# Optimization experiments

Hardware: AMD Instinct MI355X
Metric: run time of the kernel (lower is better)

Reference implementation:

```python
import jax, jax.numpy as jnp
import numpy as np

FEAT = [(200, 200), (100, 100), (50, 50), (25, 25), (13, 13)]
STRIDES = [4, 8, 16, 32, 64]
SIZES = [32, 64, 128, 256, 512]
RATIOS = np.array([0.5, 1.0, 2.0])
NUM_PER_LEVEL = [h * w * 3 for h, w in FEAT]  # [120000,30000,7500,1875,507]
A_TOTAL = sum(NUM_PER_LEVEL)                  # 159882
B = 4
IMG_H = IMG_W = 800.0
PRE_NMS = 1000      # pre_nms_top_n['testing'] (per level)
POST_NMS = 1000     # post_nms_top_n['testing']
NMS_T = 0.7
SCORE_T = 0.0
MIN_SIZE = 0.001
BBOX_CLIP = float(np.log(1000.0 / 16.0))  # torchvision bbox_xform_clip
LVL_OFFSET = 1000.0                       # > max image coord, for batched_nms trick
LVL_FULL = jnp.asarray(np.repeat(np.arange(5), NUM_PER_LEVEL))  # [A_TOTAL]


def _make_anchors():
    out = []
    for (fh, fw), stride, size in zip(FEAT, STRIDES, SIZES):
        ws = np.sqrt(size * size / RATIOS)
        hs = ws * RATIOS
        base = np.stack([-ws / 2, -hs / 2, ws / 2, hs / 2], axis=1)  # [3,4]
        sx = (np.arange(fw) + 0.5) * stride
        sy = (np.arange(fh) + 0.5) * stride
        cy, cx = np.meshgrid(sy, sx, indexing='ij')
        shifts = np.stack([cx, cy, cx, cy], axis=-1).reshape(-1, 1, 4)
        out.append((shifts + base[None]).reshape(-1, 4))
    return np.concatenate(out, 0).astype(np.float32)


def setup_inputs() -> dict:
    key = jax.random.key(0)
    k1, k2 = jax.random.split(key)
    objectness = jax.random.normal(k1, (B, A_TOTAL), jnp.float32)
    pred_bbox_deltas = jax.random.normal(k2, (B, A_TOTAL, 4), jnp.float32) * 0.5
    anchors = jnp.asarray(_make_anchors())  # real FPN anchor grid [A_TOTAL,4]
    return {"objectness": objectness, "pred_bbox_deltas": pred_bbox_deltas, "anchors": anchors}


def _decode(deltas, anchors):
    # torchvision BoxCoder.decode with weights (1,1,1,1)
    wa = anchors[:, 2] - anchors[:, 0]
    ha = anchors[:, 3] - anchors[:, 1]
    cxa = anchors[:, 0] + 0.5 * wa
    cya = anchors[:, 1] + 0.5 * ha
    dx, dy = deltas[..., 0], deltas[..., 1]
    dw = jnp.minimum(deltas[..., 2], BBOX_CLIP)
    dh = jnp.minimum(deltas[..., 3], BBOX_CLIP)
    cx = dx * wa + cxa
    cy = dy * ha + cya
    w = jnp.exp(dw) * wa
    h = jnp.exp(dh) * ha
    return jnp.stack([cx - 0.5 * w, cy - 0.5 * h, cx + 0.5 * w, cy + 0.5 * h], axis=-1)


def _pairwise_iou(b):
    area = (b[:, 2] - b[:, 0]) * (b[:, 3] - b[:, 1])
    lt = jnp.maximum(b[:, None, :2], b[None, :, :2])
    rb = jnp.minimum(b[:, None, 2:], b[None, :, 2:])
    wh = jnp.clip(rb - lt, 0.0)
    inter = wh[..., 0] * wh[..., 1]
    return inter / (area[:, None] + area[None, :] - inter)


def _nms_image(boxes, scores, lvl):
    # boxes [K,4], scores [K], lvl [K] -> fixed-size [POST_NMS,5] = (x1,y1,x2,y2,score)
    K = boxes.shape[0]
    sg = jax.lax.stop_gradient
    x1 = jnp.clip(boxes[:, 0], 0.0, IMG_W)
    y1 = jnp.clip(boxes[:, 1], 0.0, IMG_H)
    x2 = jnp.clip(boxes[:, 2], 0.0, IMG_W)
    y2 = jnp.clip(boxes[:, 3], 0.0, IMG_H)
    boxes = jnp.stack([x1, y1, x2, y2], axis=1)
    # remove_small_boxes + score threshold
    valid = (sg(x2 - x1) >= MIN_SIZE) & (sg(y2 - y1) >= MIN_SIZE) & (sg(scores) >= SCORE_T)
    order = jnp.argsort(-jnp.where(valid, sg(scores), -jnp.inf))
    boxes = boxes[order]
    scores = scores[order]
    lvl = lvl[order]
    valid = valid[order]
    # batched_nms trick: offset boxes per level so cross-level IoU is 0
    off = sg(boxes) + (lvl.astype(boxes.dtype) * LVL_OFFSET)[:, None]
    iou = _pairwise_iou(off)  # [K,K], decision-only (stop_gradient)
    idx = jnp.arange(K)
    def body(i, keep):
        sup = (iou[i] > NMS_T) & keep[i] & (idx > i)
        return keep & (~sup)
    keep = jax.lax.fori_loop(0, K, body, valid)
    rank = jnp.cumsum(keep) - 1
    sel = keep & (rank < POST_NMS)
    rows = jnp.concatenate([boxes, scores[:, None]], axis=1)
    dst = jnp.where(sel, rank, POST_NMS)  # out-of-range rows dropped
    out = jnp.zeros((POST_NMS, 5), boxes.dtype)
    return out.at[dst].set(jnp.where(sel[:, None], rows, 0.0), mode="drop")


def reference(objectness, pred_bbox_deltas, anchors):
    proposals = _decode(pred_bbox_deltas, anchors)  # [B, A_TOTAL, 4]
    # per-level top-k on objectness logits
    idx_list = []
    off = 0
    for n in NUM_PER_LEVEL:
        k = min(PRE_NMS, n)
        _, ti = jax.lax.top_k(objectness[:, off:off + n], k)
        idx_list.append(ti + off)
        off += n
    top_idx = jnp.concatenate(idx_list, axis=1)  # [B, K=4507]
    obj_k = jnp.take_along_axis(objectness, top_idx, axis=1)
    boxes_k = jnp.take_along_axis(proposals, top_idx[..., None], axis=1)
    lvl_k = LVL_FULL[top_idx]
    scores_k = jax.nn.sigmoid(obj_k)
    # clip + small-box filter + score filter + batched NMS + post-nms topk, per image
    return jax.vmap(_nms_image)(boxes_k, scores_k, lvl_k)  # [B, POST_NMS, 5]
```

## Files before the change

### kernel.cpp

```cpp
#include <hip/hip_runtime.h>
#include <stdint.h>

#define KTOT 4507
#define POSTN 1000
#define ATOT 159882
#define NIMG 4
#define CAND_CAP 4096
#define SLOTCAP 5000
#define BPI 22
#define MT_IMG 73728


__device__ inline unsigned fmono(float f) {
    unsigned u = __float_as_uint(f);
    return (u & 0x80000000u) ? ~u : (u | 0x80000000u);
}
__device__ inline float fmono_inv(unsigned u) {
    unsigned b = (u & 0x80000000u) ? (u ^ 0x80000000u) : ~u;
    return __uint_as_float(b);
}

__device__ inline unsigned long long shfl_u64(unsigned long long v, int src) {
    int lo = __shfl((int)(unsigned)(v & 0xFFFFFFFFULL), src);
    int hi = __shfl((int)(unsigned)(v >> 32), src);
    return ((unsigned long long)(unsigned)hi << 32) | (unsigned)lo;
}

__device__ inline void async16(unsigned long long* lds, const unsigned long long* g) {
#if __has_builtin(__builtin_amdgcn_global_load_lds)
    __builtin_amdgcn_global_load_lds(
        (const __attribute__((address_space(1))) unsigned*)g,
        (__attribute__((address_space(3))) unsigned*)lds, 16, 0, 0);
#else
    *(ulonglong2*)lds = *(const ulonglong2*)g;
#endif
}

__device__ inline int blockExclScan(int v, int* warpSums) {
    int tid = threadIdx.x;
    int lane = tid & 63, wid = tid >> 6;
    int x = v;
#pragma unroll
    for (int d = 1; d < 64; d <<= 1) {
        int y = __shfl_up(x, d);
        if (lane >= d) x += y;
    }
    if (lane == 63) warpSums[wid] = x;
    __syncthreads();
    if (wid == 0) {
        int s = (lane < 16) ? warpSums[lane] : 0;
#pragma unroll
        for (int d = 1; d < 16; d <<= 1) {
            int y = __shfl_up(s, d);
            if (lane >= d) s += y;
        }
        if (lane < 16) warpSums[lane] = s;
    }
    __syncthreads();
    int wpre = (wid == 0) ? 0 : warpSums[wid - 1];
    return wpre + (x - v);
}

__device__ __constant__ int c_lvlOff[5] = {0, 120000, 150000, 157500, 159375};
__device__ __constant__ int c_lvlN[5]   = {120000, 30000, 7500, 1875, 507};
__device__ __constant__ int c_slsz[5]   = {8000, 7500, 7500, 1875, 507};
__device__ __constant__ int c_blvl[BPI] = {0,0,0,0,0,0,0,0,0,0,0,0,0,0,0, 1,1,1,1, 2, 3, 4};
__device__ __constant__ int c_bsl[BPI]  = {0,1,2,3,4,5,6,7,8,9,10,11,12,13,14, 0,1,2,3, 0, 0, 0};
__device__ __constant__ int c_bstart[5] = {0, 15, 19, 20, 21};
__device__ __constant__ int c_bcnt[5]   = {15, 4, 1, 1, 1};

__device__ inline size_t mtBase(int img, int lvl) {
    return (size_t)img * MT_IMG + (lvl < 4 ? (size_t)lvl * 16384 : 65536);
}


__global__ __launch_bounds__(1024) void hist_kernel(const float* __restrict__ obj,
                                                    unsigned* __restrict__ ghist) {
    __shared__ unsigned hist[4096];
    int img = blockIdx.x / BPI, b = blockIdx.x % BPI;
    int lvl = c_blvl[b], sl = c_bsl[b];
    int n = c_lvlN[lvl];
    int s0 = sl * c_slsz[lvl];
    int send = min(s0 + c_slsz[lvl], n);
    const float* src = obj + (size_t)img * ATOT + c_lvlOff[lvl];
    int tid = threadIdx.x;

    for (int i = tid; i < 4096; i += 1024) hist[i] = 0u;
    __syncthreads();

    int base = s0 + tid, last = send - 1;
    float v0 = src[min(base,        last)];
    float v1 = src[min(base + 1024, last)];
    float v2 = src[min(base + 2048, last)];
    float v3 = src[min(base + 3072, last)];
    float v4 = src[min(base + 4096, last)];
    float v5 = src[min(base + 5120, last)];
    float v6 = src[min(base + 6144, last)];
    float v7 = src[min(base + 7168, last)];
#define HIST1(U, VV) if (base + (U)*1024 < send) atomicAdd(&hist[fmono(VV) >> 20], 1u);
    HIST1(0, v0) HIST1(1, v1) HIST1(2, v2) HIST1(3, v3)
    HIST1(4, v4) HIST1(5, v5) HIST1(6, v6) HIST1(7, v7)
#undef HIST1
    __syncthreads();

    unsigned* gh = ghist + (size_t)(img * BPI + b) * 4096;
    for (int i = tid; i < 4096; i += 1024) gh[i] = hist[i];
}


__global__ __launch_bounds__(1024) void gather_kernel(const float* __restrict__ obj,
                                                      const unsigned* __restrict__ ghist,
                                                      unsigned long long* __restrict__ gcand,
                                                      int* __restrict__ gcnt,
                                                      int* __restrict__ gbstar) {
    __shared__ int s_misc[32];
    __shared__ int s_bstar, s_cnt;
    int img = blockIdx.x / BPI, b = blockIdx.x % BPI;
    int lvl = c_blvl[b], sl = c_bsl[b];
    int seg = img * BPI + b;
    int n = c_lvlN[lvl];
    int k = (lvl == 4) ? 507 : 1000;
    int s0 = sl * c_slsz[lvl];
    int send = min(s0 + c_slsz[lvl], n);
    const float* src = obj + (size_t)img * ATOT + c_lvlOff[lvl];
    int tid = threadIdx.x;
    int lane = tid & 63;

    if (tid == 0) s_cnt = 0;

    unsigned hx = 0, hy = 0, hz = 0, hw = 0;
    {
        int bs = c_bstart[lvl], bc = c_bcnt[lvl];
        for (int s = 0; s < bc; s++) {
            const uint4* gh4 = (const uint4*)(ghist + (size_t)(img * BPI + bs + s) * 4096);
            uint4 t = gh4[tid];
            hx += t.x; hy += t.y; hz += t.z; hw += t.w;
        }
    }
    int mysum = (int)(hx + hy + hz + hw);
    int excl = blockExclScan(mysum, s_misc);
    int target = n - k;
    {
        int P = excl;
        if ((int)hx > 0 && P <= target && target < P + (int)hx) s_bstar = 4 * tid + 0;
        P += (int)hx;
        if ((int)hy > 0 && P <= target && target < P + (int)hy) s_bstar = 4 * tid + 1;
        P += (int)hy;
        if ((int)hz > 0 && P <= target && target < P + (int)hz) s_bstar = 4 * tid + 2;
        P += (int)hz;
        if ((int)hw > 0 && P <= target && target < P + (int)hw) s_bstar = 4 * tid + 3;
    }
    __syncthreads();
    int bstar = s_bstar;
    if (tid == 0 && sl == 0) gbstar[img * 5 + lvl] = bstar;

    unsigned long long* gc = gcand + (size_t)seg * CAND_CAP;
    int base = s0 + tid, last = send - 1;
    float v0 = src[min(base,        last)];
    float v1 = src[min(base + 1024, last)];
    float v2 = src[min(base + 2048, last)];
    float v3 = src[min(base + 3072, last)];
    float v4 = src[min(base + 4096, last)];
    float v5 = src[min(base + 5120, last)];
    float v6 = src[min(base + 6144, last)];
    float v7 = src[min(base + 7168, last)];
#define PUSH1(U, VV)                                                                     \
    {                                                                                    \
        int ix = base + (U) * 1024;                                                      \
        unsigned key = fmono(VV);                                                        \
        bool s = (ix < send) && ((int)(key >> 20) >= bstar);                             \
        unsigned long long mk = __ballot(s);                                             \
        if (mk) {                                                                        \
            int pre = __popcll(mk & ((1ULL << lane) - 1ULL));                            \
            int ldr = __builtin_ctzll(mk);                                               \
            int basew = 0;                                                               \
            if (lane == ldr) basew = atomicAdd(&s_cnt, __popcll(mk));                    \
            basew = __shfl(basew, ldr);                                                  \
            if (s) {                                                                     \
                int pos = basew + pre;                                                   \
                if (pos < CAND_CAP)                                                      \
                    gc[pos] = ((unsigned long long)key << 32) | (unsigned)(~(unsigned)ix); \
            }                                                                            \
        }                                                                                \
    }
    PUSH1(0, v0) PUSH1(1, v1) PUSH1(2, v2) PUSH1(3, v3)
    PUSH1(4, v4) PUSH1(5, v5) PUSH1(6, v6) PUSH1(7, v7)
#undef PUSH1
    __syncthreads();
    if (tid == 0) gcnt[seg] = min(s_cnt, CAND_CAP);
}


__global__ __launch_bounds__(1024) void rankdecode_kernel(
    const float* __restrict__ deltas, const float* __restrict__ anchors,
    const unsigned long long* __restrict__ gcand, const int* __restrict__ gcnt,
    const int* __restrict__ gbstar,
    float* __restrict__ sx1, float* __restrict__ sy1, float* __restrict__ sx2,
    float* __restrict__ sy2, float* __restrict__ sscore,
    float* __restrict__ cx1, float* __restrict__ cy1, float* __restrict__ cx2,
    float* __restrict__ cy2, float* __restrict__ car,
    unsigned long long* __restrict__ ckey, int* __restrict__ cslot, int* __restrict__ cm) {
    __shared__ unsigned long long ck[CAND_CAP];
    __shared__ __attribute__((aligned(16))) unsigned subh[4096];
    __shared__ int s_warp[32];
    __shared__ int s_tot, s_sub, s_m2;

    int grp = blockIdx.x;
    int img = grp / 5, lvl = grp % 5;
    int kn = (lvl == 4) ? 507 : 1000;
    int koff = lvl * 1000;
    int tid = threadIdx.x;

    int bs = c_bstart[lvl], bc = c_bcnt[lvl];
    int pref = 0;
    for (int s = 0; s < bc; s++) {
        int c = gcnt[img * BPI + bs + s];
        const unsigned long long* segp = gcand + (size_t)(img * BPI + bs + s) * CAND_CAP;
        for (int i = tid; i < c; i += 1024) {
            int d = pref + i;
            if (d < CAND_CAP) ck[d] = segp[i];
        }
        pref += c;
    }
    int m = min(pref, CAND_CAP);
    int bstarv = gbstar[grp];
    __syncthreads();

    int mm = m;
    if (m > 1024) {
        for (int i = tid; i < 4096; i += 1024) subh[i] = 0u;
        __syncthreads();
        int c0 = tid, c1 = tid + 1024, c2 = tid + 2048, c3 = tid + 3072;
        unsigned long long e0 = (c0 < m) ? ck[c0] : 0ULL;
        unsigned long long e1 = (c1 < m) ? ck[c1] : 0ULL;
        unsigned long long e2 = (c2 < m) ? ck[c2] : 0ULL;
        unsigned long long e3 = (c3 < m) ? ck[c3] : 0ULL;
        int hiCnt = 0;
#define CLS(E, C)                                                                        \
        if ((C) < m) {                                                                   \
            if ((unsigned)((E) >> 52) > (unsigned)bstarv) hiCnt++;                       \
            else atomicAdd(&subh[(unsigned)(((E) >> 40) & 0xFFFULL)], 1u);               \
        }
        CLS(e0, c0) CLS(e1, c1) CLS(e2, c2) CLS(e3, c3)
#undef CLS
        int exH = blockExclScan(hiCnt, s_warp);
        if (tid == 1023) s_tot = exH + hiCnt;
        __syncthreads();
        int cntHi = s_tot;
        int target2 = (m - cntHi) - (kn - cntHi);
        const uint4* sh4 = (const uint4*)subh;
        uint4 sc = sh4[tid];
        int ms2 = (int)(sc.x + sc.y + sc.z + sc.w);
        int ex2 = blockExclScan(ms2, s_warp);
        {
            int Pp = ex2;
            if ((int)sc.x > 0 && Pp <= target2 && target2 < Pp + (int)sc.x) s_sub = 4 * tid + 0;
            Pp += (int)sc.x;
            if ((int)sc.y > 0 && Pp <= target2 && target2 < Pp + (int)sc.y) s_sub = 4 * tid + 1;
            Pp += (int)sc.y;
            if ((int)sc.z > 0 && Pp <= target2 && target2 < Pp + (int)sc.z) s_sub = 4 * tid + 2;
            Pp += (int)sc.z;
            if ((int)sc.w > 0 && Pp <= target2 && target2 < Pp + (int)sc.w) s_sub = 4 * tid + 3;
        }
        __syncthreads();
        int cstar = s_sub;
#define FLG(E, C)                                                                        \
        (((C) < m) && (((unsigned)((E) >> 52) > (unsigned)bstarv) ||                     \
                       ((unsigned)(((E) >> 40) & 0xFFFULL) >= (unsigned)cstar)))
        int f0 = FLG(e0, c0), f1 = FLG(e1, c1), f2 = FLG(e2, c2), f3 = FLG(e3, c3);
#undef FLG
        int fc = f0 + f1 + f2 + f3;
        int pos = blockExclScan(fc, s_warp);
        if (tid == 1023) s_m2 = pos + fc;
        __syncthreads();
        int m2 = s_m2;
        if (m2 <= 1024) {
            int p = pos;
            if (f0) ck[p++] = e0;
            if (f1) ck[p++] = e1;
            if (f2) ck[p++] = e2;
            if (f3) ck[p++] = e3;
            mm = m2;
        }
        __syncthreads();
    }

    int P = 512;
    while (P < mm) P <<= 1;
    for (int i = mm + tid; i < P; i += 1024) ck[i] = 0ULL;
    __syncthreads();

    for (unsigned kk = 2; kk <= (unsigned)P; kk <<= 1) {
        for (unsigned j = kk >> 1; j > 0; j >>= 1) {
            for (unsigned i = (unsigned)tid; i < (unsigned)P; i += 1024) {
                unsigned ixj = i ^ j;
                if (ixj > i) {
                    unsigned long long a = ck[i], b2 = ck[ixj];
                    bool up = ((i & kk) == 0);
                    if ((a > b2) == up) { ck[i] = b2; ck[ixj] = a; }
                }
            }
            __syncthreads();
        }
    }

    int r = tid;
    size_t o = (size_t)img * KTOT + koff + r;
    float x1 = 0.f, y1 = 0.f, x2 = 0.f, y2 = 0.f, s = 0.f;
    int valid = 0;
    if (r < kn) {
        unsigned long long key = ck[P - 1 - r];
        int idx = c_lvlOff[lvl] + (int)(~(unsigned)key);
        float logit = fmono_inv((unsigned)(key >> 32));
        float ef = (float)exp(-(double)logit);
        s = 1.0f / __fadd_rn(1.0f, ef);
        float a0 = anchors[(size_t)idx * 4 + 0], a1 = anchors[(size_t)idx * 4 + 1];
        float a2 = anchors[(size_t)idx * 4 + 2], a3 = anchors[(size_t)idx * 4 + 3];
        const float* dp = deltas + ((size_t)img * ATOT + idx) * 4;
        float dx = dp[0], dy = dp[1];
        const float BCLIP = 4.135166556742356f;
        float dw = fminf(dp[2], BCLIP), dh = fminf(dp[3], BCLIP);
        float wa = __fsub_rn(a2, a0), ha = __fsub_rn(a3, a1);
        float cxa = __fadd_rn(a0, __fmul_rn(0.5f, wa));
        float cya = __fadd_rn(a1, __fmul_rn(0.5f, ha));
        float cx = __fadd_rn(__fmul_rn(dx, wa), cxa);
        float cy = __fadd_rn(__fmul_rn(dy, ha), cya);
        float w = __fmul_rn((float)exp((double)dw), wa);
        float h = __fmul_rn((float)exp((double)dh), ha);
        x1 = __fsub_rn(cx, __fmul_rn(0.5f, w));
        y1 = __fsub_rn(cy, __fmul_rn(0.5f, h));
        x2 = __fadd_rn(cx, __fmul_rn(0.5f, w));
        y2 = __fadd_rn(cy, __fmul_rn(0.5f, h));
        x1 = fminf(fmaxf(x1, 0.0f), 800.0f);
        y1 = fminf(fmaxf(y1, 0.0f), 800.0f);
        x2 = fminf(fmaxf(x2, 0.0f), 800.0f);
        y2 = fminf(fmaxf(y2, 0.0f), 800.0f);
        valid = (__fsub_rn(x2, x1) >= 0.001f) && (__fsub_rn(y2, y1) >= 0.001f) && (s >= 0.0f);
        sx1[o] = x1; sy1[o] = y1; sx2[o] = x2; sy2[o] = y2; sscore[o] = s;
    }

    int pos = blockExclScan(valid, s_warp);
    if (valid) {
        float lf = 1000.0f * (float)lvl;
        size_t cb = (size_t)img * SLOTCAP + koff + pos;
        float ox1 = __fadd_rn(x1, lf);
        float oy1 = __fadd_rn(y1, lf);
        float ox2 = __fadd_rn(x2, lf);
        float oy2 = __fadd_rn(y2, lf);
        cx1[cb] = ox1; cy1[cb] = oy1; cx2[cb] = ox2; cy2[cb] = oy2;
        car[cb] = __fmul_rn(__fsub_rn(ox2, ox1), __fsub_rn(oy2, oy1));
        int p = koff + r;
        ckey[cb] = ((unsigned long long)fmono(s) << 32) | (unsigned)(~(unsigned)p);
        cslot[cb] = p;
    }
    if (tid == 1023) cm[grp] = pos + valid;
}


__global__ __launch_bounds__(512) void mask_kernel(
    const float* __restrict__ cx1, const float* __restrict__ cy1,
    const float* __restrict__ cx2, const float* __restrict__ cy2,
    const float* __restrict__ car, const int* __restrict__ cm,
    unsigned long long* __restrict__ maskT) {
    __shared__ float lx1[1000], ly1[1000], lx2[1000], ly2[1000], lar[1000];
    int iq = blockIdx.y;
    int img = iq / 5, lvl = iq % 5;
    int m = cm[iq];
    int W = (m + 63) >> 6;
    int T = (W * (W + 1)) >> 1;
    int tbase = blockIdx.x * 8;
    if (tbase >= T) return;

    size_t cb0 = (size_t)img * SLOTCAP + lvl * 1000;
    for (int q = threadIdx.x; q < m; q += 512) {
        lx1[q] = cx1[cb0 + q]; ly1[q] = cy1[cb0 + q];
        lx2[q] = cx2[cb0 + q]; ly2[q] = cy2[cb0 + q];
        lar[q] = car[cb0 + q];
    }
    __syncthreads();

    int wv = threadIdx.x >> 6, lane = threadIdx.x & 63;
    int t = tbase + wv;
    if (t >= T) return;
    int w = (int)((sqrtf(8.0f * (float)t + 1.0f) - 1.0f) * 0.5f);
    while (((w + 1) * (w + 2)) / 2 <= t) w++;
    while ((w * (w + 1)) / 2 > t) w--;
    int c = t - ((w * (w + 1)) >> 1);

    unsigned long long* MT = maskT + mtBase(img, lvl);

    int j = (w << 6) + lane;
    bool jv = j < m;
    float jx1 = jv ? lx1[j] : 0.f, jy1 = jv ? ly1[j] : 0.f;
    float jx2 = jv ? lx2[j] : 0.f, jy2 = jv ? ly2[j] : 0.f;
    float jar = jv ? lar[j] : 0.f;

    unsigned long long myword = 0ULL;
    int i0 = c << 6, i1 = min(i0 + 64, m);
    for (int i = i0; i < i1; i++) {
        float ix1 = lx1[i], iy1 = ly1[i], ix2 = lx2[i], iy2 = ly2[i], iar = lar[i];
        float ltx = fmaxf(ix1, jx1);
        float lty = fmaxf(iy1, jy1);
        float rbx = fminf(ix2, jx2);
        float rby = fminf(iy2, jy2);
        float wq = fmaxf(__fsub_rn(rbx, ltx), 0.0f);
        float hq = fmaxf(__fsub_rn(rby, lty), 0.0f);
        float inter = __fmul_rn(wq, hq);
        float uni = __fsub_rn(__fadd_rn(iar, jar), inter);
        float iou = inter / uni;
        bool bit = jv && (j > i) && (iou > 0.7f);
        unsigned long long bal = __ballot(bit);
        if (lane == (i & 63)) myword = bal;
    }
    int irow = i0 + lane;
    if (irow < i1) MT[(size_t)irow * 16 + w] = myword;
}


__global__ __launch_bounds__(256, 1) void scan_kernel(
    const unsigned long long* __restrict__ maskT, const int* __restrict__ cm,
    unsigned long long* __restrict__ keepWords) {
    __shared__ unsigned long long M[16384];
    __shared__ unsigned long long s_alive[16], s_kill[16];
    __shared__ int s_go;
    int grp = blockIdx.x;
    int img = grp / 5, lvl = grp % 5;
    int m = cm[grp];
    int tid = threadIdx.x;
    int wv = tid >> 6, lane = tid & 63;
    int w16 = lane & 15, g = lane >> 4;
    int rowgrp = wv * 4 + g;

    if (m == 0) {
        if (tid < 16) keepWords[grp * 16 + tid] = 0ULL;
        return;
    }

    const unsigned long long* src = maskT + mtBase(img, lvl);
    int rounds = (m * 16 + 511) >> 9;
    for (int k = 0; k < rounds; k++) {
        int u = (k << 9) + tid * 2;
        async16(&M[u], &src[u]);
    }
    int fw = m >> 6, tb = m & 63;
    if (tid < 16) {
        unsigned long long a = (tid < fw) ? ~0ULL
                              : (tid == fw && tb) ? ((1ULL << tb) - 1ULL) : 0ULL;
        s_alive[tid] = a;
        s_kill[tid] = 0ULL;
    }
    if (tid == 0) s_go = 1;
    __syncthreads();

    for (int it = 0; it <= m && s_go; it++) {
        unsigned long long p = 0ULL;
        for (int r = rowgrp; r < m; r += 16) {
            unsigned long long aw = s_alive[r >> 6];
            unsigned long long bit = (aw >> (r & 63)) & 1ULL;
            bit &= (unsigned long long)(w16 >= (r >> 6));
            p |= M[r * 16 + w16] & (0ULL - bit);
        }
        p |= shfl_u64(p, (lane + 32) & 63);
        p |= shfl_u64(p, (lane + 16) & 63);
        if (lane < 16 && p) atomicOr(&s_kill[lane], p);
        __syncthreads();
        if (wv == 0) {
            unsigned long long neww = 0ULL, oldw = 0ULL;
            if (lane < 16) {
                unsigned long long initw = (lane < fw) ? ~0ULL
                                          : (lane == fw && tb) ? ((1ULL << tb) - 1ULL) : 0ULL;
                oldw = s_alive[lane];
                neww = initw & ~s_kill[lane];
                s_alive[lane] = neww;
                s_kill[lane] = 0ULL;
            }
            unsigned long long ch = __ballot(lane < 16 && neww != oldw);
            if (lane == 0) s_go = (ch != 0ULL) ? 1 : 0;
        }
        __syncthreads();
    }
    if (tid < 16) keepWords[grp * 16 + tid] = s_alive[tid];
}


__global__ __launch_bounds__(1024) void scanout_kernel(
    const float* __restrict__ sx1, const float* __restrict__ sy1,
    const float* __restrict__ sx2, const float* __restrict__ sy2,
    const float* __restrict__ sscore,
    const unsigned long long* __restrict__ ckey, const int* __restrict__ cslot,
    const unsigned long long* __restrict__ keepWords, float* __restrict__ out) {
    __shared__ unsigned long long kkey[SLOTCAP];
    __shared__ int kslot[SLOTCAP];
    __shared__ int s_warp[32];
    __shared__ int s_pref[6];
    __shared__ int s_cnt[5];

    int img = blockIdx.x, tid = threadIdx.x;

    int f[5];
    int e0 = tid * 5;
    int cnt = 0;
#pragma unroll
    for (int c = 0; c < 5; c++) {
        int e = e0 + c;
        int fl = 0;
        if (e < 5000) {
            int lvl = e / 1000, rr = e - lvl * 1000;
            fl = (int)((keepWords[(img * 5 + lvl) * 16 + (rr >> 6)] >> (rr & 63)) & 1ULL);
        }
        f[c] = fl;
        cnt += fl;
    }
    int pos = blockExclScan(cnt, s_warp);
    {
        int run = pos;
#pragma unroll
        for (int c = 0; c < 5; c++) {
            int e = e0 + c;
            if (e < 5000 && (e - (e / 1000) * 1000) == 0) s_pref[e / 1000] = run;
            run += f[c];
        }
    }
    if (tid == 1023) s_pref[5] = pos + cnt;
    __syncthreads();
    {
        int run = pos;
#pragma unroll
        for (int c = 0; c < 5; c++) {
            int e = e0 + c;
            if (f[c]) {
                int lvl = e / 1000, rr = e - lvl * 1000;
                int pil = run - s_pref[lvl];
                size_t cb = (size_t)img * SLOTCAP + lvl * 1000 + rr;
                kkey[lvl * 1000 + pil] = ckey[cb];
                kslot[lvl * 1000 + pil] = cslot[cb];
            }
            run += f[c];
        }
    }
    if (tid < 5) s_cnt[tid] = s_pref[tid + 1] - s_pref[tid];
    __syncthreads();

    int tK = s_pref[5];

    for (int lvl = 0; lvl < 5; lvl++) {
        int Kc = s_cnt[lvl];
        int koff = lvl * 1000;
        for (int q = tid; q < Kc; q += 1024) {
            unsigned long long key = kkey[koff + q];
            int rank = q;
#pragma unroll
            for (int ol = 0; ol < 5; ol++) {
                if (ol == lvl) continue;
                int lo = 0, hi = s_cnt[ol], base = ol * 1000;
                while (lo < hi) {
                    int mid = (lo + hi) >> 1;
                    if (kkey[base + mid] > key) lo = mid + 1; else hi = mid;
                }
                rank += lo;
            }
            if (rank < POSTN) {
                int slot = kslot[koff + q];
                size_t o = (size_t)img * KTOT + slot;
                float* dst = out + ((size_t)img * POSTN + rank) * 5;
                dst[0] = sx1[o]; dst[1] = sy1[o]; dst[2] = sx2[o]; dst[3] = sy2[o];
                dst[4] = sscore[o];
            }
        }
    }

    int z0 = tK < POSTN ? tK : POSTN;
    int nz = (POSTN - z0) * 5;
    float* ob = out + (size_t)img * POSTN * 5 + (size_t)z0 * 5;
    for (int u = tid; u < nz; u += 1024) ob[u] = 0.f;
}


extern "C" void kernel_launch(void* const* d_in, const int* in_sizes, int n_in,
                              void* d_out, int out_size, void* d_ws, size_t ws_size,
                              hipStream_t stream) {
    const float* obj = (const float*)d_in[0];
    const float* deltas = (const float*)d_in[1];
    const float* anchors = (const float*)d_in[2];
    float* out = (float*)d_out;

    char* ws = (char*)d_ws;
    size_t off = 0;
    auto alloc = [&](size_t bytes) {
        size_t o = off;
        off += (bytes + 255) & ~(size_t)255;
        return o;
    };
    unsigned* ghist = (unsigned*)(ws + alloc((size_t)NIMG * BPI * 4096 * 4));
    int* gcnt = (int*)(ws + alloc((size_t)NIMG * BPI * 4));
    int* gbstar = (int*)(ws + alloc((size_t)NIMG * 5 * 4));
    unsigned long long* gcand =
        (unsigned long long*)(ws + alloc((size_t)NIMG * BPI * CAND_CAP * 8));
    float* sx1 = (float*)(ws + alloc((size_t)NIMG * KTOT * 4));
    float* sy1 = (float*)(ws + alloc((size_t)NIMG * KTOT * 4));
    float* sx2 = (float*)(ws + alloc((size_t)NIMG * KTOT * 4));
    float* sy2 = (float*)(ws + alloc((size_t)NIMG * KTOT * 4));
    float* sscore = (float*)(ws + alloc((size_t)NIMG * KTOT * 4));
    float* cx1 = (float*)(ws + alloc((size_t)NIMG * SLOTCAP * 4));
    float* cy1 = (float*)(ws + alloc((size_t)NIMG * SLOTCAP * 4));
    float* cx2 = (float*)(ws + alloc((size_t)NIMG * SLOTCAP * 4));
    float* cy2 = (float*)(ws + alloc((size_t)NIMG * SLOTCAP * 4));
    float* car = (float*)(ws + alloc((size_t)NIMG * SLOTCAP * 4));
    unsigned long long* ckey = (unsigned long long*)(ws + alloc((size_t)NIMG * SLOTCAP * 8));
    int* cslot = (int*)(ws + alloc((size_t)NIMG * SLOTCAP * 4));
    int* cm = (int*)(ws + alloc((size_t)NIMG * 5 * 4));
    unsigned long long* maskT = (unsigned long long*)(ws + alloc((size_t)NIMG * MT_IMG * 8));
    unsigned long long* keepWords = (unsigned long long*)(ws + alloc((size_t)NIMG * 5 * 16 * 8));

    hist_kernel<<<dim3(NIMG * BPI), dim3(1024), 0, stream>>>(obj, ghist);
    gather_kernel<<<dim3(NIMG * BPI), dim3(1024), 0, stream>>>(obj, ghist, gcand, gcnt,
                                                               gbstar);
    rankdecode_kernel<<<dim3(NIMG * 5), dim3(1024), 0, stream>>>(
        deltas, anchors, gcand, gcnt, gbstar, sx1, sy1, sx2, sy2, sscore,
        cx1, cy1, cx2, cy2, car, ckey, cslot, cm);
    mask_kernel<<<dim3(17, NIMG * 5), dim3(512), 0, stream>>>(cx1, cy1, cx2, cy2, car, cm,
                                                              maskT);
    scan_kernel<<<dim3(NIMG * 5), dim3(256), 0, stream>>>(maskT, cm, keepWords);
    scanout_kernel<<<dim3(NIMG), dim3(1024), 0, stream>>>(
        sx1, sy1, sx2, sy2, sscore, ckey, cslot, keepWords, out);
}
```

Baseline: 163.1 us.

## Fuse rank/decode, IoU mask build, and NMS scan into one per-level kernel

Measured after the change: 265.7 us. 62.9% more time.

```diff
diff --git a/kernel.cpp b/kernel.cpp
--- a/kernel.cpp
+++ b/kernel.cpp
@@ -8,7 +8,6 @@
 #define CAND_CAP 4096
 #define SLOTCAP 5000
 #define BPI 22
-#define MT_IMG 73728
 
 
 __device__ inline unsigned fmono(float f) {
@@ -24,16 +23,6 @@
     int lo = __shfl((int)(unsigned)(v & 0xFFFFFFFFULL), src);
     int hi = __shfl((int)(unsigned)(v >> 32), src);
     return ((unsigned long long)(unsigned)hi << 32) | (unsigned)lo;
-}
-
-__device__ inline void async16(unsigned long long* lds, const unsigned long long* g) {
-#if __has_builtin(__builtin_amdgcn_global_load_lds)
-    __builtin_amdgcn_global_load_lds(
-        (const __attribute__((address_space(1))) unsigned*)g,
-        (__attribute__((address_space(3))) unsigned*)lds, 16, 0, 0);
-#else
-    *(ulonglong2*)lds = *(const ulonglong2*)g;
-#endif
 }
 
 __device__ inline int blockExclScan(int v, int* warpSums) {
@@ -68,10 +57,6 @@
 __device__ __constant__ int c_bsl[BPI]  = {0,1,2,3,4,5,6,7,8,9,10,11,12,13,14, 0,1,2,3, 0, 0, 0};
 __device__ __constant__ int c_bstart[5] = {0, 15, 19, 20, 21};
 __device__ __constant__ int c_bcnt[5]   = {15, 4, 1, 1, 1};
-
-__device__ inline size_t mtBase(int img, int lvl) {
-    return (size_t)img * MT_IMG + (lvl < 4 ? (size_t)lvl * 16384 : 65536);
-}
 
 
 __global__ __launch_bounds__(1024) void hist_kernel(const float* __restrict__ obj,
@@ -191,25 +176,29 @@
 }
 
 
-__global__ __launch_bounds__(1024) void rankdecode_kernel(
+__global__ __launch_bounds__(1024, 1) void mega_kernel(
     const float* __restrict__ deltas, const float* __restrict__ anchors,
     const unsigned long long* __restrict__ gcand, const int* __restrict__ gcnt,
     const int* __restrict__ gbstar,
     float* __restrict__ sx1, float* __restrict__ sy1, float* __restrict__ sx2,
     float* __restrict__ sy2, float* __restrict__ sscore,
-    float* __restrict__ cx1, float* __restrict__ cy1, float* __restrict__ cx2,
-    float* __restrict__ cy2, float* __restrict__ car,
-    unsigned long long* __restrict__ ckey, int* __restrict__ cslot, int* __restrict__ cm) {
-    __shared__ unsigned long long ck[CAND_CAP];
-    __shared__ __attribute__((aligned(16))) unsigned subh[4096];
+    unsigned long long* __restrict__ ckey, int* __restrict__ cslot,
+    unsigned long long* __restrict__ keepWords) {
+    __shared__ __attribute__((aligned(16))) unsigned long long M[16384];
+    __shared__ float lx1[1024], ly1[1024], lx2[1024], ly2[1024], lar[1024];
     __shared__ int s_warp[32];
-    __shared__ int s_tot, s_sub, s_m2;
+    __shared__ unsigned long long s_alive[16], s_kill[16];
+    __shared__ int s_go, s_m, s_tot, s_sub, s_m2;
+
+    unsigned long long* ck = M;
+    unsigned* subh = (unsigned*)(M + 4096);
 
     int grp = blockIdx.x;
     int img = grp / 5, lvl = grp % 5;
     int kn = (lvl == 4) ? 507 : 1000;
     int koff = lvl * 1000;
     int tid = threadIdx.x;
+    int wv = tid >> 6, lane = tid & 63;
 
     int bs = c_bstart[lvl], bc = c_bcnt[lvl];
     int pref = 0;
@@ -247,7 +236,7 @@
         if (tid == 1023) s_tot = exH + hiCnt;
         __syncthreads();
         int cntHi = s_tot;
-        int target2 = (m - cntHi) - (kn - cntHi);
+        int target2 = m - kn;
         const uint4* sh4 = (const uint4*)subh;
         uint4 sc = sh4[tid];
         int ms2 = (int)(sc.x + sc.y + sc.z + sc.w);
@@ -269,6 +258,7 @@
                        ((unsigned)(((E) >> 40) & 0xFFFULL) >= (unsigned)cstar)))
         int f0 = FLG(e0, c0), f1 = FLG(e1, c1), f2 = FLG(e2, c2), f3 = FLG(e3, c3);
 #undef FLG
+        (void)cntHi;
         int fc = f0 + f1 + f2 + f3;
         int pos = blockExclScan(fc, s_warp);
         if (tid == 1023) s_m2 = pos + fc;
@@ -289,7 +279,6 @@
     while (P < mm) P <<= 1;
     for (int i = mm + tid; i < P; i += 1024) ck[i] = 0ULL;
     __syncthreads();
-
     for (unsigned kk = 2; kk <= (unsigned)P; kk <<= 1) {
         for (unsigned j = kk >> 1; j > 0; j >>= 1) {
             for (unsigned i = (unsigned)tid; i < (unsigned)P; i += 1024) {
@@ -338,127 +327,81 @@
         valid = (__fsub_rn(x2, x1) >= 0.001f) && (__fsub_rn(y2, y1) >= 0.001f) && (s >= 0.0f);
         sx1[o] = x1; sy1[o] = y1; sx2[o] = x2; sy2[o] = y2; sscore[o] = s;
     }
-
     int pos = blockExclScan(valid, s_warp);
     if (valid) {
         float lf = 1000.0f * (float)lvl;
-        size_t cb = (size_t)img * SLOTCAP + koff + pos;
         float ox1 = __fadd_rn(x1, lf);
         float oy1 = __fadd_rn(y1, lf);
         float ox2 = __fadd_rn(x2, lf);
         float oy2 = __fadd_rn(y2, lf);
-        cx1[cb] = ox1; cy1[cb] = oy1; cx2[cb] = ox2; cy2[cb] = oy2;
-        car[cb] = __fmul_rn(__fsub_rn(ox2, ox1), __fsub_rn(oy2, oy1));
+        lx1[pos] = ox1; ly1[pos] = oy1; lx2[pos] = ox2; ly2[pos] = oy2;
+        lar[pos] = __fmul_rn(__fsub_rn(ox2, ox1), __fsub_rn(oy2, oy1));
         int p = koff + r;
+        size_t cb = (size_t)img * SLOTCAP + koff + pos;
         ckey[cb] = ((unsigned long long)fmono(s) << 32) | (unsigned)(~(unsigned)p);
         cslot[cb] = p;
     }
-    if (tid == 1023) cm[grp] = pos + valid;
-}
-
-
-__global__ __launch_bounds__(512) void mask_kernel(
-    const float* __restrict__ cx1, const float* __restrict__ cy1,
-    const float* __restrict__ cx2, const float* __restrict__ cy2,
-    const float* __restrict__ car, const int* __restrict__ cm,
-    unsigned long long* __restrict__ maskT) {
-    __shared__ float lx1[1000], ly1[1000], lx2[1000], ly2[1000], lar[1000];
-    int iq = blockIdx.y;
-    int img = iq / 5, lvl = iq % 5;
-    int m = cm[iq];
-    int W = (m + 63) >> 6;
-    int T = (W * (W + 1)) >> 1;
-    int tbase = blockIdx.x * 8;
-    if (tbase >= T) return;
-
-    size_t cb0 = (size_t)img * SLOTCAP + lvl * 1000;
-    for (int q = threadIdx.x; q < m; q += 512) {
-        lx1[q] = cx1[cb0 + q]; ly1[q] = cy1[cb0 + q];
-        lx2[q] = cx2[cb0 + q]; ly2[q] = cy2[cb0 + q];
-        lar[q] = car[cb0 + q];
-    }
-    __syncthreads();
-
-    int wv = threadIdx.x >> 6, lane = threadIdx.x & 63;
-    int t = tbase + wv;
-    if (t >= T) return;
-    int w = (int)((sqrtf(8.0f * (float)t + 1.0f) - 1.0f) * 0.5f);
-    while (((w + 1) * (w + 2)) / 2 <= t) w++;
-    while ((w * (w + 1)) / 2 > t) w--;
-    int c = t - ((w * (w + 1)) >> 1);
-
-    unsigned long long* MT = maskT + mtBase(img, lvl);
-
-    int j = (w << 6) + lane;
-    bool jv = j < m;
-    float jx1 = jv ? lx1[j] : 0.f, jy1 = jv ? ly1[j] : 0.f;
-    float jx2 = jv ? lx2[j] : 0.f, jy2 = jv ? ly2[j] : 0.f;
-    float jar = jv ? lar[j] : 0.f;
-
-    unsigned long long myword = 0ULL;
-    int i0 = c << 6, i1 = min(i0 + 64, m);
-    for (int i = i0; i < i1; i++) {
-        float ix1 = lx1[i], iy1 = ly1[i], ix2 = lx2[i], iy2 = ly2[i], iar = lar[i];
-        float ltx = fmaxf(ix1, jx1);
-        float lty = fmaxf(iy1, jy1);
-        float rbx = fminf(ix2, jx2);
-        float rby = fminf(iy2, jy2);
-        float wq = fmaxf(__fsub_rn(rbx, ltx), 0.0f);
-        float hq = fmaxf(__fsub_rn(rby, lty), 0.0f);
-        float inter = __fmul_rn(wq, hq);
-        float uni = __fsub_rn(__fadd_rn(iar, jar), inter);
-        float iou = inter / uni;
-        bool bit = jv && (j > i) && (iou > 0.7f);
-        unsigned long long bal = __ballot(bit);
-        if (lane == (i & 63)) myword = bal;
-    }
-    int irow = i0 + lane;
-    if (irow < i1) MT[(size_t)irow * 16 + w] = myword;
-}
-
-
-__global__ __launch_bounds__(256, 1) void scan_kernel(
-    const unsigned long long* __restrict__ maskT, const int* __restrict__ cm,
-    unsigned long long* __restrict__ keepWords) {
-    __shared__ unsigned long long M[16384];
-    __shared__ unsigned long long s_alive[16], s_kill[16];
-    __shared__ int s_go;
-    int grp = blockIdx.x;
-    int img = grp / 5, lvl = grp % 5;
-    int m = cm[grp];
-    int tid = threadIdx.x;
-    int wv = tid >> 6, lane = tid & 63;
-    int w16 = lane & 15, g = lane >> 4;
-    int rowgrp = wv * 4 + g;
-
-    if (m == 0) {
+    if (tid == 1023) s_m = pos + valid;
+    __syncthreads();
+
+    int mv = s_m;
+    if (mv == 0) {
         if (tid < 16) keepWords[grp * 16 + tid] = 0ULL;
         return;
     }
-
-    const unsigned long long* src = maskT + mtBase(img, lvl);
-    int rounds = (m * 16 + 511) >> 9;
-    for (int k = 0; k < rounds; k++) {
-        int u = (k << 9) + tid * 2;
-        async16(&M[u], &src[u]);
-    }
-    int fw = m >> 6, tb = m & 63;
+    int W = (mv + 63) >> 6;
+    int T = (W * (W + 1)) >> 1;
+
+    for (int t = wv; t < T; t += 16) {
+        int w = (int)((sqrtf(8.0f * (float)t + 1.0f) - 1.0f) * 0.5f);
+        while (((w + 1) * (w + 2)) / 2 <= t) w++;
+        while ((w * (w + 1)) / 2 > t) w--;
+        int c = t - ((w * (w + 1)) >> 1);
+
+        int j = (w << 6) + lane;
+        bool jv = j < mv;
+        float jx1 = jv ? lx1[j] : 0.f, jy1 = jv ? ly1[j] : 0.f;
+        float jx2 = jv ? lx2[j] : 0.f, jy2 = jv ? ly2[j] : 0.f;
+        float jar = jv ? lar[j] : 0.f;
+
+        unsigned long long myword = 0ULL;
+        int i0 = c << 6, i1 = min(i0 + 64, mv);
+        for (int i = i0; i < i1; i++) {
+            float ix1 = lx1[i], iy1 = ly1[i], ix2 = lx2[i], iy2 = ly2[i], iar = lar[i];
+            float ltx = fmaxf(ix1, jx1);
+            float lty = fmaxf(iy1, jy1);
+            float rbx = fminf(ix2, jx2);
+            float rby = fminf(iy2, jy2);
+            float wq = fmaxf(__fsub_rn(rbx, ltx), 0.0f);
+            float hq = fmaxf(__fsub_rn(rby, lty), 0.0f);
+            float inter = __fmul_rn(wq, hq);
+            float uni = __fsub_rn(__fadd_rn(iar, jar), inter);
+            float iou = inter / uni;
+            bool bit = jv && (j > i) && (iou > 0.7f);
+            unsigned long long bal = __ballot(bit);
+            if (lane == (i & 63)) myword = bal;
+        }
+        int irow = i0 + lane;
+        if (irow < i1) M[irow * 16 + w] = myword;
+    }
+
+    int w16 = lane & 15, g = lane >> 4;
+    int rowcls = wv * 4 + g;
+    int fw = mv >> 6, tb = mv & 63;
     if (tid < 16) {
-        unsigned long long a = (tid < fw) ? ~0ULL
-                              : (tid == fw && tb) ? ((1ULL << tb) - 1ULL) : 0ULL;
-        s_alive[tid] = a;
+        s_alive[tid] = (tid < fw) ? ~0ULL : (tid == fw && tb) ? ((1ULL << tb) - 1ULL) : 0ULL;
         s_kill[tid] = 0ULL;
     }
     if (tid == 0) s_go = 1;
     __syncthreads();
 
-    for (int it = 0; it <= m && s_go; it++) {
+    for (int it = 0; it <= mv && s_go; it++) {
         unsigned long long p = 0ULL;
-        for (int r = rowgrp; r < m; r += 16) {
-            unsigned long long aw = s_alive[r >> 6];
-            unsigned long long bit = (aw >> (r & 63)) & 1ULL;
-            bit &= (unsigned long long)(w16 >= (r >> 6));
-            p |= M[r * 16 + w16] & (0ULL - bit);
+        for (int rr = rowcls; rr < mv; rr += 64) {
+            unsigned long long aw = s_alive[rr >> 6];
+            unsigned long long bit = (aw >> (rr & 63)) & 1ULL;
+            bit &= (unsigned long long)(w16 >= (rr >> 6));
+            p |= M[rr * 16 + w16] & (0ULL - bit);
         }
         p |= shfl_u64(p, (lane + 32) & 63);
         p |= shfl_u64(p, (lane + 16) & 63);
@@ -601,26 +544,16 @@
     float* sx2 = (float*)(ws + alloc((size_t)NIMG * KTOT * 4));
     float* sy2 = (float*)(ws + alloc((size_t)NIMG * KTOT * 4));
     float* sscore = (float*)(ws + alloc((size_t)NIMG * KTOT * 4));
-    float* cx1 = (float*)(ws + alloc((size_t)NIMG * SLOTCAP * 4));
-    float* cy1 = (float*)(ws + alloc((size_t)NIMG * SLOTCAP * 4));
-    float* cx2 = (float*)(ws + alloc((size_t)NIMG * SLOTCAP * 4));
-    float* cy2 = (float*)(ws + alloc((size_t)NIMG * SLOTCAP * 4));
-    float* car = (float*)(ws + alloc((size_t)NIMG * SLOTCAP * 4));
     unsigned long long* ckey = (unsigned long long*)(ws + alloc((size_t)NIMG * SLOTCAP * 8));
     int* cslot = (int*)(ws + alloc((size_t)NIMG * SLOTCAP * 4));
-    int* cm = (int*)(ws + alloc((size_t)NIMG * 5 * 4));
-    unsigned long long* maskT = (unsigned long long*)(ws + alloc((size_t)NIMG * MT_IMG * 8));
     unsigned long long* keepWords = (unsigned long long*)(ws + alloc((size_t)NIMG * 5 * 16 * 8));
 
     hist_kernel<<<dim3(NIMG * BPI), dim3(1024), 0, stream>>>(obj, ghist);
     gather_kernel<<<dim3(NIMG * BPI), dim3(1024), 0, stream>>>(obj, ghist, gcand, gcnt,
                                                                gbstar);
-    rankdecode_kernel<<<dim3(NIMG * 5), dim3(1024), 0, stream>>>(
+    mega_kernel<<<dim3(NIMG * 5), dim3(1024), 0, stream>>>(
         deltas, anchors, gcand, gcnt, gbstar, sx1, sy1, sx2, sy2, sscore,
-        cx1, cy1, cx2, cy2, car, ckey, cslot, cm);
-    mask_kernel<<<dim3(17, NIMG * 5), dim3(512), 0, stream>>>(cx1, cy1, cx2, cy2, car, cm,
-                                                              maskT);
-    scan_kernel<<<dim3(NIMG * 5), dim3(256), 0, stream>>>(maskT, cm, keepWords);
+        ckey, cslot, keepWords);
     scanout_kernel<<<dim3(NIMG), dim3(1024), 0, stream>>>(
         sx1, sy1, sx2, sy2, sscore, ckey, cslot, keepWords, out);
 }
```
